# Kernel optimization log

Measured on AMD Instinct MI355X. Metric: run time of the kernel, lower is better.

Reference implementation:

```python
import jax, jax.numpy as jnp
import numpy as np

LEAK = 0.1
K = 16  # nsample


def _gather(points, idx):
    # points: [B, N2, C], idx: [B, N1, K] -> [B, N1, K, C]
    return jax.vmap(lambda p, i: p[i])(points, idx)


def setup_inputs() -> dict:
    key = jax.random.key(0)
    ks = jax.random.split(key, 32)
    B, N1, N2, C = 2, 4096, 8192, 64
    M = [64, 64, 64]
    d = {}
    d['xyz1'] = jax.random.normal(ks[0], (B, 3, N1), dtype=jnp.float32)
    d['xyz2'] = jax.random.normal(ks[1], (B, 3, N2), dtype=jnp.float32)
    d['points1'] = jax.random.normal(ks[2], (B, C, N1), dtype=jnp.float32)
    d['points2'] = jax.random.normal(ks[3], (B, C, N2), dtype=jnp.float32)
    d['knn1'] = jax.random.normal(ks[4], (B, C, N1), dtype=jnp.float32)
    d['knn2'] = jax.random.normal(ks[5], (B, C, N2), dtype=jnp.float32)
    s = 0.05
    # fuse 1x1 Conv1d weights (no bias): [out=M0, in=C]
    for j, nm in enumerate(['Wfr', 'Wfro', 'Wfz', 'Wfr2', 'Wfro2', 'Wfz2']):
        d[nm] = jax.random.normal(ks[6 + j], (M[0], C), dtype=jnp.float32) * s
    # mlp 1x1 Conv2d weights/biases: layer0 in=3, then M[i-1]
    ins = [3, M[0], M[1]]
    k = 12
    for br in ['r', 'z', 'h']:
        for i in range(3):
            d['W%s%d' % (br, i)] = jax.random.normal(ks[k], (M[i], ins[i]), dtype=jnp.float32) * s
            d['b%s%d' % (br, i)] = jax.random.normal(ks[k + 1], (M[i],), dtype=jnp.float32) * s
            k += 2
    return d


def _forward(xyz1, xyz2, points1, points2, knn1, knn2,
             Wfr, Wfro, Wfz, Wfr2, Wfro2, Wfz2,
             Wr0, br0, Wr1, br1, Wr2, br2,
             Wz0, bz0, Wz1, bz1, Wz2, bz2,
             Wh0, bh0, Wh1, bh1, Wh2, bh2):
    leaky = lambda x: jax.nn.leaky_relu(x, LEAK)
    conv = lambda x, W, b: jnp.einsum('bnkc,oc->bnko', x, W) + b
    fuse = lambda p, W: jnp.einsum('oc,bcn->bno', W, p)  # [B,N,Cout]

    x1 = jnp.transpose(xyz1, (0, 2, 1))   # [B,N1,3]
    x2 = jnp.transpose(xyz2, (0, 2, 1))   # [B,N2,3]
    f1 = jnp.transpose(knn1, (0, 2, 1))   # [B,N1,Ck]
    f2 = jnp.transpose(knn2, (0, 2, 1))   # [B,N2,Ck]

    # cosine knn on feature space (smallest distance = largest similarity)
    f1n = f1 / jnp.sqrt(jnp.sum(f1 * f1, -1, keepdims=True) + 1e-8)
    f2n = f2 / jnp.sqrt(jnp.sum(f2 * f2, -1, keepdims=True) + 1e-8)
    cdist = 1.0 - jnp.einsum('bnc,bmc->bnm', f1n, f2n)
    _, idx_c = jax.lax.top_k(-cdist, K // 2)
    # euclidean knn on xyz
    sq = (jnp.sum(x1 * x1, -1)[:, :, None] + jnp.sum(x2 * x2, -1)[:, None, :]
          - 2.0 * jnp.einsum('bnc,bmc->bnm', x1, x2))
    _, idx_p = jax.lax.top_k(-sq, K // 2)
    idx = jnp.concatenate([idx_c, idx_p], axis=-1)  # [B,N1,K]

    p2r = fuse(points2, Wfr2)    # [B,N2,M0]
    p2ro = fuse(points2, Wfro2)
    p2z = fuse(points2, Wfz2)
    g_r = _gather(p2r, idx)      # [B,N1,K,M0]
    g_ro = _gather(p2ro, idx)
    g_z = _gather(p2z, idx)
    dirx = _gather(x2, idx) - x1[:, :, None, :]  # [B,N1,K,3]

    # r gate
    gp1r = fuse(points1, Wfr)[:, :, None, :]
    r = leaky(conv(dirx, Wr0, br0) + gp1r + g_r)
    r = leaky(conv(r, Wr1, br1))
    r = jax.nn.sigmoid(conv(r, Wr2, br2))          # [B,N1,K,M2]

    # z gate (max over K before last layer)
    gp1z = fuse(points1, Wfz)[:, :, None, :]
    z = leaky(conv(dirx, Wz0, bz0) + gp1z + g_ro)
    z = jnp.max(leaky(conv(z, Wz1, bz1)), axis=2, keepdims=True)
    z = jax.nn.sigmoid(conv(z, Wz2, bz2))[:, :, 0, :]  # [B,N1,M2]

    # h candidate; note: original code's `if self.relu:` is always truthy
    # (self.relu holds the LeakyReLU module), so final activation is LeakyReLU.
    p1o = fuse(points1, Wfro)                       # [B,N1,M0]
    p1e = r * p1o[:, :, None, :]
    h = leaky(conv(dirx, Wh0, bh0) + p1e + g_z)
    h = jnp.max(leaky(conv(h, Wh1, bh1)), axis=2, keepdims=True)
    h = leaky(conv(h, Wh2, bh2))[:, :, 0, :]        # [B,N1,M2]

    out = (1.0 - z) * p1o + z * h                   # [B,N1,M2]
    return jnp.transpose(out, (0, 2, 1))            # [B,M2,N1]


def reference(xyz1, xyz2, points1, points2, knn1, knn2,
              Wfr, Wfro, Wfz, Wfr2, Wfro2, Wfz2,
              Wr0, br0, Wr1, br1, Wr2, br2,
              Wz0, bz0, Wz1, bz1, Wz2, bz2,
              Wh0, bh0, Wh1, bh1, Wh2, bh2):
    return _forward(xyz1, xyz2, points1, points2, knn1, knn2,
                    Wfr, Wfro, Wfz, Wfr2, Wfro2, Wfz2,
                    Wr0, br0, Wr1, br1, Wr2, br2,
                    Wz0, bz0, Wz1, bz1, Wz2, bz2,
                    Wh0, bh0, Wh1, bh1, Wh2, bh2)
```

## Files before the change

### kernel.cpp

```cpp
#include <hip/hip_runtime.h>
#include <math.h>

#define NB 2
#define NN1 4096
#define NN2 8192
#define NPART 16
#define PARTSZ (NN2 / NPART)
#define NCHUNK (PARTSZ / 128)
#define LEAKK 0.1f
#define GPAD 68

typedef unsigned long long u64k;

__device__ __forceinline__ float leaky_(float x) { return fmaxf(x, LEAKK * x); }
__device__ __forceinline__ float sigm_(float x) { return 1.0f / (1.0f + __expf(-x)); }

__device__ __forceinline__ void insq_(u64k k, u64k* q) {
#pragma unroll
  for (int j = 7; j > 0; --j)
    q[j] = (k < q[j - 1]) ? q[j - 1] : ((k < q[j]) ? k : q[j]);
  q[0] = (k < q[0]) ? k : q[0];
}

__device__ __forceinline__ void merge8q_(u64k* a, u64k* b) {
  u64k r[8];
#pragma unroll
  for (int s = 0; s < 8; ++s) {
    bool ta = a[0] < b[0];
    r[s] = ta ? a[0] : b[0];
#pragma unroll
    for (int j = 0; j < 7; ++j) {
      a[j] = ta ? a[j + 1] : a[j];
      b[j] = ta ? b[j] : b[j + 1];
    }
  }
#pragma unroll
  for (int j = 0; j < 8; ++j) a[j] = r[j];
}

__global__ void prep_w_kernel(const float* s0, const float* s1, const float* s2,
                              const float* s3, const float* s4, const float* s5,
                              const float* s6, const float* s7, const float* s8,
                              const float* s9, const float* s10, const float* s11,
                              const float* s12, const float* s13, const float* s14,
                              float* wt) {
  const float* srcs[15] = {s0, s1, s2, s3, s4, s5, s6, s7, s8, s9, s10, s11, s12, s13, s14};
  int bid = blockIdx.x;
  const float* src = srcs[bid];
  int cols = (bid < 6) ? 64 : (((bid - 6) % 3 == 0) ? 3 : 64);
  float* dst = wt + bid * 4096;
  for (int e = threadIdx.x; e < 64 * cols; e += blockDim.x) {
    int o = e / cols, c = e - o * cols;
    dst[c * 64 + o] = src[e];
  }
}

__global__ __launch_bounds__(256) void prep_side_kernel(const float* knn, const float* xyz,
                                                        float* fdst, float* xdst, int N) {
  __shared__ float T[64 * 65];
  __shared__ float ps[4 * 64];
  int b = blockIdx.y;
  int n0 = blockIdx.x * 64;
  int t = threadIdx.x, w = t >> 6, l = t & 63;
  const float* kb = knn + (size_t)b * 64 * N + n0;
#pragma unroll
  for (int i = 0; i < 16; ++i) {
    int c = w * 16 + i;
    T[c * 65 + l] = kb[(size_t)c * N + l];
  }
  __syncthreads();
  float s = 0.f;
#pragma unroll
  for (int i = 0; i < 16; ++i) { float v = T[(w * 16 + i) * 65 + l]; s += v * v; }
  ps[w * 64 + l] = s;
  __syncthreads();
#pragma unroll
  for (int i = 0; i < 16; ++i) {
    int p = w * 16 + i;
    float rsum = ps[p] + ps[64 + p] + ps[128 + p] + ps[192 + p];
    float rs = 1.0f / sqrtf(rsum + 1e-8f);
    fdst[(size_t)(b * N + n0 + p) * 64 + l] = T[l * 65 + p] * rs;
  }
  if (t < 64) {
    const float* xb = xyz + (size_t)b * 3 * N + n0;
    float x = xb[t], y = xb[N + t], z = xb[2 * N + t];
    ((float4*)xdst)[b * N + n0 + t] = make_float4(x, y, z, x * x + y * y + z * z);
  }
}

__global__ __launch_bounds__(256) void fuse_kernel(const float* pts, const float* wt0,
                                                   const float* wt1, const float* wt2,
                                                   float* d0, float* d1, float* d2, int N) {
  int b = blockIdx.y;
  int w = threadIdx.x >> 6, l = threadIdx.x & 63;
  int n = blockIdx.x * 4 + w;
  const float* pb = pts + (size_t)b * 64 * N + n;
  float a0 = 0.f, a1 = 0.f, a2 = 0.f;
  for (int c = 0; c < 64; ++c) {
    float p = pb[(size_t)c * N];
    a0 += p * wt0[c * 64 + l];
    a1 += p * wt1[c * 64 + l];
    a2 += p * wt2[c * 64 + l];
  }
  size_t ob = (size_t)(b * N + n) * 64 + l;
  d0[ob] = a0; d1[ob] = a1; d2[ob] = a2;
}

__global__ __launch_bounds__(256, 3) void knn_kernel(const float* f1n, const float* f2n,
                                                     const float* x1t, const float* x2t,
                                                     u64k* pq) {
  __shared__ __align__(16) float SH[13120];
  float* f1t = SH;
  float* f2d = SH + 4096;
  float* x1x = SH + 12352;
  float* x1y = SH + 12416;
  float* x1z = SH + 12480;
  float* x1w = SH + 12544;
  float* x2s = SH + 12608;

  int t = threadIdx.x;
  int lane = t & 63, w = t >> 6;
  int n0 = blockIdx.x * 64;
  int part = (int)blockIdx.y;
  int b = (int)blockIdx.z;

  {
    const float* f1row = f1n + (size_t)(b * NN1 + n0 + lane) * 64;
#pragma unroll
    for (int pass = 0; pass < 4; ++pass) {
      int c0 = pass * 16 + w * 4;
      float4 v = *(const float4*)(f1row + c0);
      f1t[(c0 + 0) * 64 + lane] = v.x;
      f1t[(c0 + 1) * 64 + lane] = v.y;
      f1t[(c0 + 2) * 64 + lane] = v.z;
      f1t[(c0 + 3) * 64 + lane] = v.w;
    }
    if (t < 64) {
      float4 v = ((const float4*)x1t)[b * NN1 + n0 + t];
      x1x[t] = v.x; x1y[t] = v.y; x1z[t] = v.z; x1w[t] = v.w;
    }
  }

  u64k cq[8], eq[8];
#pragma unroll
  for (int j = 0; j < 8; ++j) { cq[j] = ~0ull; eq[j] = ~0ull; }

  int ty = t >> 4, tx = t & 15;
  __syncthreads();
  float xx = x1x[lane], xy = x1y[lane], xz = x1z[lane], xw = x1w[lane];

  for (int ch = 0; ch < NCHUNK; ++ch) {
    int cc = part * PARTSZ + ch * 128;

    {
      int cand = t & 127;
      int sb = (t >> 7) * 8;
      const float* src = f2n + (size_t)(b * NN2 + cc + cand) * 64 + sb * 4;
#pragma unroll
      for (int p = 0; p < 8; ++p) {
        float4 v = *(const float4*)(src + p * 4);
        int c0 = (sb + p) * 4;
        f2d[(c0 + 0) * 128 + cand] = v.x;
        f2d[(c0 + 1) * 128 + cand] = v.y;
        f2d[(c0 + 2) * 128 + cand] = v.z;
        f2d[(c0 + 3) * 128 + cand] = v.w;
      }
      if (t < 128) ((float4*)x2s)[t] = ((const float4*)x2t)[b * NN2 + cc + t];
    }
    __syncthreads();

    float acc0[4][4], acc1[4][4];
#pragma unroll
    for (int i = 0; i < 4; ++i)
#pragma unroll
      for (int j = 0; j < 4; ++j) { acc0[i][j] = 0.f; acc1[i][j] = 0.f; }

#pragma unroll 2
    for (int k = 0; k < 64; ++k) {
      float4 a  = *(const float4*)&f1t[k * 64 + ty * 4];
      float4 b0 = *(const float4*)&f2d[k * 128 + tx * 4];
      float4 b1 = *(const float4*)&f2d[k * 128 + 64 + tx * 4];
      acc0[0][0] += a.x * b0.x; acc0[0][1] += a.x * b0.y; acc0[0][2] += a.x * b0.z; acc0[0][3] += a.x * b0.w;
      acc0[1][0] += a.y * b0.x; acc0[1][1] += a.y * b0.y; acc0[1][2] += a.y * b0.z; acc0[1][3] += a.y * b0.w;
      acc0[2][0] += a.z * b0.x; acc0[2][1] += a.z * b0.y; acc0[2][2] += a.z * b0.z; acc0[2][3] += a.z * b0.w;
      acc0[3][0] += a.w * b0.x; acc0[3][1] += a.w * b0.y; acc0[3][2] += a.w * b0.z; acc0[3][3] += a.w * b0.w;
      acc1[0][0] += a.x * b1.x; acc1[0][1] += a.x * b1.y; acc1[0][2] += a.x * b1.z; acc1[0][3] += a.x * b1.w;
      acc1[1][0] += a.y * b1.x; acc1[1][1] += a.y * b1.y; acc1[1][2] += a.y * b1.z; acc1[1][3] += a.y * b1.w;
      acc1[2][0] += a.z * b1.x; acc1[2][1] += a.z * b1.y; acc1[2][2] += a.z * b1.z; acc1[2][3] += a.z * b1.w;
      acc1[3][0] += a.w * b1.x; acc1[3][1] += a.w * b1.y; acc1[3][2] += a.w * b1.z; acc1[3][3] += a.w * b1.w;
    }
    __syncthreads();

#pragma unroll
    for (int i = 0; i < 4; ++i) {
      int r = ty * 4 + i;
#pragma unroll
      for (int j = 0; j < 4; ++j) {
        f2d[r * 129 + tx * 4 + j]      = fmaxf(1.f - acc0[i][j], 0.f);
        f2d[r * 129 + 64 + tx * 4 + j] = fmaxf(1.f - acc1[i][j], 0.f);
      }
    }
    __syncthreads();

    {
      const float* drow = &f2d[lane * 129 + w * 32];
      const float4* x2q = ((const float4*)x2s) + w * 32;
#pragma unroll 4
      for (int j = 0; j < 32; ++j) {
        unsigned gi = cc + w * 32 + j;
        float dv = drow[j];
        u64k kc = ((u64k)__float_as_uint(dv) << 32) | gi;
        if (kc < cq[7]) insq_(kc, cq);
        float4 xv = x2q[j];
        float d3 = fmaxf(xw + xv.w - 2.f * (xx * xv.x + xy * xv.y + xz * xv.z), 0.f);
        u64k ke = ((u64k)__float_as_uint(d3) << 32) | gi;
        if (ke < eq[7]) insq_(ke, eq);
      }
    }
    __syncthreads();
  }

  {
    u64k* Lc = (u64k*)SH;
    u64k* Le = ((u64k*)SH) + 2112;
#pragma unroll
    for (int j = 0; j < 8; ++j) {
      Lc[lane * 33 + w * 8 + j] = cq[j];
      Le[lane * 33 + w * 8 + j] = eq[j];
    }
    __syncthreads();
    if (t < 128) {
      int typ = t >> 6, r = t & 63;
      const u64k* L = typ ? Le : Lc;
      u64k a0[8], a1[8], a2[8], a3[8];
#pragma unroll
      for (int j = 0; j < 8; ++j) {
        a0[j] = L[r * 33 + 0 + j];
        a1[j] = L[r * 33 + 8 + j];
        a2[j] = L[r * 33 + 16 + j];
        a3[j] = L[r * 33 + 24 + j];
      }
      merge8q_(a0, a1);
      merge8q_(a2, a3);
      merge8q_(a0, a2);
      size_t base = ((size_t)((b * NPART + part) * NN1) + n0 + r) * 16 + typ * 8;
#pragma unroll
      for (int j = 0; j < 8; ++j) pq[base + j] = a0[j];
    }
  }
}

__device__ __forceinline__ void loadq_(const u64k* pq, int b, int p, int n1, int typ, u64k* q) {
  size_t base = ((size_t)((b * NPART + p) * NN1) + n1) * 16 + typ * 8;
#pragma unroll
  for (int j = 0; j < 8; ++j) q[j] = pq[base + j];
}

__global__ __launch_bounds__(256) void merge_parts_kernel(const u64k* pq, int* idxb) {
  int g = blockIdx.x * blockDim.x + threadIdx.x;
  if (g >= NB * NN1) return;
  int b = g / NN1, n1 = g - b * NN1;
  for (int typ = 0; typ < 2; ++typ) {
    u64k A[8], B[8];
    loadq_(pq, b, 0, n1, typ, A);
    for (int p = 1; p < NPART; ++p) {
      loadq_(pq, b, p, n1, typ, B);
      merge8q_(A, B);
    }
    size_t ob = (size_t)g * 16 + typ * 8;
#pragma unroll
    for (int j = 0; j < 8; ++j) idxb[ob + j] = (int)(A[j] & 0xffffffffull);
  }
}

__device__ __forceinline__ void gemm64_(const float* Ain, const float* Wt,
                                        int ty, int tx, float acc[4][4]) {
#pragma unroll
  for (int i = 0; i < 4; ++i)
#pragma unroll
    for (int j = 0; j < 4; ++j) acc[i][j] = 0.f;
#pragma unroll 8
  for (int c = 0; c < 64; ++c) {
    float4 a  = *(const float4*)&Ain[c * GPAD + ty * 4];
    float4 wv = *(const float4*)&Wt[c * 64 + tx * 4];
    acc[0][0] += a.x * wv.x; acc[0][1] += a.x * wv.y; acc[0][2] += a.x * wv.z; acc[0][3] += a.x * wv.w;
    acc[1][0] += a.y * wv.x; acc[1][1] += a.y * wv.y; acc[1][2] += a.y * wv.z; acc[1][3] += a.y * wv.w;
    acc[2][0] += a.z * wv.x; acc[2][1] += a.z * wv.y; acc[2][2] += a.z * wv.z; acc[2][3] += a.z * wv.w;
    acc[3][0] += a.w * wv.x; acc[3][1] += a.w * wv.y; acc[3][2] += a.w * wv.z; acc[3][3] += a.w * wv.w;
  }
}

__global__ __launch_bounds__(256, 4) void gru_kernel(
    const int* idxb, const float* x1t, const float* x2t,
    const float* p1r, const float* p1ro, const float* p1z,
    const float* p2r, const float* p2ro, const float* p2z,
    const float* wt,
    const float* br0, const float* br1, const float* br2,
    const float* bz0, const float* bz1, const float* bz2,
    const float* bh0, const float* bh1, const float* bh2,
    float* out) {
  __shared__ __align__(16) float A1[64 * GPAD];
  __shared__ __align__(16) float A2[64 * GPAD];
  __shared__ float Vpart[16 * 64];
  __shared__ float dxs[64 * 4];
  __shared__ int idxs[64];

  int t = threadIdx.x;
  int w = t >> 6, l = t & 63;
  int ty = t >> 4, tx = t & 15;
  int b = blockIdx.y;
  int n1i = blockIdx.x * 4 + w;
  int rowbase = b * NN1 + n1i;

  if (l < 16) {
    int gi = idxb[(size_t)rowbase * 16 + l];
    idxs[w * 16 + l] = gi;
    float4 x1v = ((const float4*)x1t)[rowbase];
    float4 x2v = ((const float4*)x2t)[b * NN2 + gi];
    dxs[(w * 16 + l) * 4 + 0] = x2v.x - x1v.x;
    dxs[(w * 16 + l) * 4 + 1] = x2v.y - x1v.y;
    dxs[(w * 16 + l) * 4 + 2] = x2v.z - x1v.z;
    dxs[(w * 16 + l) * 4 + 3] = 0.f;
  }
  float pr  = p1r [(size_t)rowbase * 64 + l];
  float pro = p1ro[(size_t)rowbase * 64 + l];
  float pz  = p1z [(size_t)rowbase * 64 + l];

  const float* Wr0t = wt + 6 * 4096;
  const float* Wr1t = wt + 7 * 4096;
  const float* Wr2t = wt + 8 * 4096;
  const float* Wz0t = wt + 9 * 4096;
  const float* Wz1t = wt + 10 * 4096;
  const float* Wz2t = wt + 11 * 4096;
  const float* Wh0t = wt + 12 * 4096;
  const float* Wh1t = wt + 13 * 4096;
  const float* Wh2t = wt + 14 * 4096;

  __syncthreads();

  {
    float w0 = Wr0t[l], w1 = Wr0t[64 + l], w2 = Wr0t[128 + l], b0 = br0[l];
#pragma unroll
    for (int k = 0; k < 16; ++k) {
      int row = w * 16 + k;
      int gi = idxs[row];
      float g = p2r[((size_t)b * NN2 + gi) * 64 + l];
      float4 d = *(const float4*)&dxs[row * 4];
      A1[l * GPAD + row] = leaky_(b0 + pr + g + w0 * d.x + w1 * d.y + w2 * d.z);
    }
  }
  __syncthreads();

  float acc[4][4];

  gemm64_(A1, Wr1t, ty, tx, acc);
  {
    const float* bq = &br1[tx * 4];
#pragma unroll
    for (int j = 0; j < 4; ++j) {
      float bb = bq[j];
#pragma unroll
      for (int i = 0; i < 4; ++i)
        A2[(tx * 4 + j) * GPAD + ty * 4 + i] = leaky_(acc[i][j] + bb);
    }
  }
  __syncthreads();

  gemm64_(A2, Wr2t, ty, tx, acc);
  {
    const float* bq = &br2[tx * 4];
#pragma unroll
    for (int j = 0; j < 4; ++j) {
      float bb = bq[j];
#pragma unroll
      for (int i = 0; i < 4; ++i)
        A1[(tx * 4 + j) * GPAD + ty * 4 + i] = sigm_(acc[i][j] + bb);
    }
  }
  __syncthreads();

  {
    float w0 = Wz0t[l], w1 = Wz0t[64 + l], w2 = Wz0t[128 + l], b0 = bz0[l];
#pragma unroll
    for (int k = 0; k < 16; ++k) {
      int row = w * 16 + k;
      int gi = idxs[row];
      float g = p2ro[((size_t)b * NN2 + gi) * 64 + l];
      float4 d = *(const float4*)&dxs[row * 4];
      A2[l * GPAD + row] = leaky_(b0 + pz + g + w0 * d.x + w1 * d.y + w2 * d.z);
    }
  }
  __syncthreads();

  gemm64_(A2, Wz1t, ty, tx, acc);
  {
    const float* bq = &bz1[tx * 4];
#pragma unroll
    for (int j = 0; j < 4; ++j) {
      float bb = bq[j];
      float m = leaky_(acc[0][j] + bb);
      m = fmaxf(m, leaky_(acc[1][j] + bb));
      m = fmaxf(m, leaky_(acc[2][j] + bb));
      m = fmaxf(m, leaky_(acc[3][j] + bb));
      Vpart[ty * 64 + tx * 4 + j] = m;
    }
  }
  __syncthreads();
  float vm;
  {
    float v0 = Vpart[(w * 4 + 0) * 64 + l];
    float v1 = Vpart[(w * 4 + 1) * 64 + l];
    float v2 = Vpart[(w * 4 + 2) * 64 + l];
    float v3 = Vpart[(w * 4 + 3) * 64 + l];
    vm = fmaxf(fmaxf(v0, v1), fmaxf(v2, v3));
  }
  __syncthreads();
  float* Vv = Vpart;
  Vv[w * 64 + l] = vm;
  __syncthreads();
  float z3;
  {
    float a = bz2[l];
#pragma unroll 8
    for (int c = 0; c < 64; ++c) a += Vv[w * 64 + c] * Wz2t[c * 64 + l];
    z3 = sigm_(a);
  }

  {
    float w0 = Wh0t[l], w1 = Wh0t[64 + l], w2 = Wh0t[128 + l], b0 = bh0[l];
#pragma unroll
    for (int k = 0; k < 16; ++k) {
      int row = w * 16 + k;
      int gi = idxs[row];
      float g = p2z[((size_t)b * NN2 + gi) * 64 + l];
      float4 d = *(const float4*)&dxs[row * 4];
      float r3 = A1[l * GPAD + row];
      A2[l * GPAD + row] = leaky_(b0 + r3 * pro + g + w0 * d.x + w1 * d.y + w2 * d.z);
    }
  }
  __syncthreads();

  gemm64_(A2, Wh1t, ty, tx, acc);
  {
    const float* bq = &bh1[tx * 4];
#pragma unroll
    for (int j = 0; j < 4; ++j) {
      float bb = bq[j];
      float m = leaky_(acc[0][j] + bb);
      m = fmaxf(m, leaky_(acc[1][j] + bb));
      m = fmaxf(m, leaky_(acc[2][j] + bb));
      m = fmaxf(m, leaky_(acc[3][j] + bb));
      Vpart[ty * 64 + tx * 4 + j] = m;
    }
  }
  __syncthreads();
  {
    float v0 = Vpart[(w * 4 + 0) * 64 + l];
    float v1 = Vpart[(w * 4 + 1) * 64 + l];
    float v2 = Vpart[(w * 4 + 2) * 64 + l];
    float v3 = Vpart[(w * 4 + 3) * 64 + l];
    vm = fmaxf(fmaxf(v0, v1), fmaxf(v2, v3));
  }
  __syncthreads();
  Vv[w * 64 + l] = vm;
  __syncthreads();
  float h3;
  {
    float a = bh2[l];
#pragma unroll 8
    for (int c = 0; c < 64; ++c) a += Vv[w * 64 + c] * Wh2t[c * 64 + l];
    h3 = leaky_(a);
  }

  out[((size_t)b * 64 + l) * NN1 + n1i] = (1.0f - z3) * pro + z3 * h3;
}

extern "C" void kernel_launch(void* const* d_in, const int* in_sizes, int n_in,
                              void* d_out, int out_size, void* d_ws, size_t ws_size,
                              hipStream_t stream) {
  (void)in_sizes; (void)n_in; (void)out_size; (void)ws_size;
  const float* xyz1    = (const float*)d_in[0];
  const float* xyz2    = (const float*)d_in[1];
  const float* points1 = (const float*)d_in[2];
  const float* points2 = (const float*)d_in[3];
  const float* knn1    = (const float*)d_in[4];
  const float* knn2    = (const float*)d_in[5];
  const float* Wfr   = (const float*)d_in[6];
  const float* Wfro  = (const float*)d_in[7];
  const float* Wfz   = (const float*)d_in[8];
  const float* Wfr2  = (const float*)d_in[9];
  const float* Wfro2 = (const float*)d_in[10];
  const float* Wfz2  = (const float*)d_in[11];
  const float* Wr0 = (const float*)d_in[12]; const float* br0 = (const float*)d_in[13];
  const float* Wr1 = (const float*)d_in[14]; const float* br1 = (const float*)d_in[15];
  const float* Wr2 = (const float*)d_in[16]; const float* br2 = (const float*)d_in[17];
  const float* Wz0 = (const float*)d_in[18]; const float* bz0 = (const float*)d_in[19];
  const float* Wz1 = (const float*)d_in[20]; const float* bz1 = (const float*)d_in[21];
  const float* Wz2 = (const float*)d_in[22]; const float* bz2 = (const float*)d_in[23];
  const float* Wh0 = (const float*)d_in[24]; const float* bh0 = (const float*)d_in[25];
  const float* Wh1 = (const float*)d_in[26]; const float* bh1 = (const float*)d_in[27];
  const float* Wh2 = (const float*)d_in[28]; const float* bh2 = (const float*)d_in[29];

  float* W = (float*)d_ws;
  size_t o = 0;
  float* f1n = W + o; o += (size_t)NB * NN1 * 64;
  float* f2n = W + o; o += (size_t)NB * NN2 * 64;
  float* x1t = W + o; o += (size_t)NB * NN1 * 4;
  float* x2t = W + o; o += (size_t)NB * NN2 * 4;
  float* p1r = W + o; o += (size_t)NB * NN1 * 64;
  float* p1ro = W + o; o += (size_t)NB * NN1 * 64;
  float* p1z = W + o; o += (size_t)NB * NN1 * 64;
  float* p2r = W + o; o += (size_t)NB * NN2 * 64;
  float* p2ro = W + o; o += (size_t)NB * NN2 * 64;
  float* p2z = W + o; o += (size_t)NB * NN2 * 64;
  float* wt = W + o; o += (size_t)15 * 4096;
  u64k* pq = (u64k*)(W + o); o += (size_t)2 * NB * NPART * NN1 * 16;
  int* idxb = (int*)(W + o); o += (size_t)NB * NN1 * 16;

  float* out = (float*)d_out;

  hipLaunchKernelGGL(prep_w_kernel, dim3(15), dim3(256), 0, stream,
                     Wfr, Wfro, Wfz, Wfr2, Wfro2, Wfz2,
                     Wr0, Wr1, Wr2, Wz0, Wz1, Wz2, Wh0, Wh1, Wh2, wt);
  hipLaunchKernelGGL(prep_side_kernel, dim3(NN1 / 64, NB), dim3(256), 0, stream,
                     knn1, xyz1, f1n, x1t, NN1);
  hipLaunchKernelGGL(prep_side_kernel, dim3(NN2 / 64, NB), dim3(256), 0, stream,
                     knn2, xyz2, f2n, x2t, NN2);
  hipLaunchKernelGGL(fuse_kernel, dim3(NN1 / 4, NB), dim3(256), 0, stream,
                     points1, wt + 0 * 4096, wt + 1 * 4096, wt + 2 * 4096,
                     p1r, p1ro, p1z, NN1);
  hipLaunchKernelGGL(fuse_kernel, dim3(NN2 / 4, NB), dim3(256), 0, stream,
                     points2, wt + 3 * 4096, wt + 4 * 4096, wt + 5 * 4096,
                     p2r, p2ro, p2z, NN2);
  hipLaunchKernelGGL(knn_kernel, dim3(NN1 / 64, NPART, NB), dim3(256), 0, stream,
                     f1n, f2n, x1t, x2t, pq);
  hipLaunchKernelGGL(merge_parts_kernel, dim3((NB * NN1 + 255) / 256), dim3(256), 0, stream,
                     pq, idxb);
  hipLaunchKernelGGL(gru_kernel, dim3(NN1 / 4, NB), dim3(256), 0, stream,
                     idxb, x1t, x2t, p1r, p1ro, p1z, p2r, p2ro, p2z, wt,
                     br0, br1, br2, bz0, bz1, bz2, bh0, bh1, bh2, out);
}
```

Measured before the change: 578.9 us.

## Store normalized features channel-major and use branchless float top-k insertion

The prep kernel now writes the normalized knn features in channel-major layout, so the knn kernel loads its shared-memory tiles with direct float4 copies instead of scattered transposing stores. The per-candidate top-8 insertion switches from conditional 64-bit key compare-and-insert to a branchless float/int min-max network, and packs to sortable 64-bit keys only at merge time. The clamping of distances to zero is removed; the sign-aware packing is meant to keep the ordering correct for negative values. The branchless insert runs on every candidate rather than only those that beat the current worst, which trades the early-out for no divergence and more ALU work per candidate.

```diff
diff --git a/kernel.cpp b/kernel.cpp
--- a/kernel.cpp
+++ b/kernel.cpp
@@ -15,11 +15,23 @@
 __device__ __forceinline__ float leaky_(float x) { return fmaxf(x, LEAKK * x); }
 __device__ __forceinline__ float sigm_(float x) { return 1.0f / (1.0f + __expf(-x)); }
 
-__device__ __forceinline__ void insq_(u64k k, u64k* q) {
-#pragma unroll
-  for (int j = 7; j > 0; --j)
-    q[j] = (k < q[j - 1]) ? q[j - 1] : ((k < q[j]) ? k : q[j]);
-  q[0] = (k < q[0]) ? k : q[0];
+__device__ __forceinline__ void insfi_(float d, int i, float* q, int* qi) {
+  bool c0 = d < q[0], c1 = d < q[1], c2 = d < q[2], c3 = d < q[3];
+  bool c4 = d < q[4], c5 = d < q[5], c6 = d < q[6], c7 = d < q[7];
+  q[7] = fminf(fmaxf(d, q[6]), q[7]);  qi[7] = c6 ? qi[6] : (c7 ? i : qi[7]);
+  q[6] = fminf(fmaxf(d, q[5]), q[6]);  qi[6] = c5 ? qi[5] : (c6 ? i : qi[6]);
+  q[5] = fminf(fmaxf(d, q[4]), q[5]);  qi[5] = c4 ? qi[4] : (c5 ? i : qi[5]);
+  q[4] = fminf(fmaxf(d, q[3]), q[4]);  qi[4] = c3 ? qi[3] : (c4 ? i : qi[4]);
+  q[3] = fminf(fmaxf(d, q[2]), q[3]);  qi[3] = c2 ? qi[2] : (c3 ? i : qi[3]);
+  q[2] = fminf(fmaxf(d, q[1]), q[2]);  qi[2] = c1 ? qi[1] : (c2 ? i : qi[2]);
+  q[1] = fminf(fmaxf(d, q[0]), q[1]);  qi[1] = c0 ? qi[0] : (c1 ? i : qi[1]);
+  q[0] = fminf(d, q[0]);               qi[0] = c0 ? i : qi[0];
+}
+
+__device__ __forceinline__ u64k packdi_(float d, int i) {
+  unsigned b = __float_as_uint(d);
+  b ^= (unsigned)(((int)b >> 31)) | 0x80000000u;
+  return ((u64k)b << 32) | (unsigned)i;
 }
 
 __device__ __forceinline__ void merge8q_(u64k* a, u64k* b) {
@@ -56,9 +68,10 @@
 }
 
 __global__ __launch_bounds__(256) void prep_side_kernel(const float* knn, const float* xyz,
-                                                        float* fdst, float* xdst, int N) {
+                                                        float* fT, float* xdst, int N) {
   __shared__ float T[64 * 65];
   __shared__ float ps[4 * 64];
+  __shared__ float rsS[64];
   int b = blockIdx.y;
   int n0 = blockIdx.x * 64;
   int t = threadIdx.x, w = t >> 6, l = t & 63;
@@ -74,17 +87,19 @@
   for (int i = 0; i < 16; ++i) { float v = T[(w * 16 + i) * 65 + l]; s += v * v; }
   ps[w * 64 + l] = s;
   __syncthreads();
-#pragma unroll
-  for (int i = 0; i < 16; ++i) {
-    int p = w * 16 + i;
-    float rsum = ps[p] + ps[64 + p] + ps[128 + p] + ps[192 + p];
-    float rs = 1.0f / sqrtf(rsum + 1e-8f);
-    fdst[(size_t)(b * N + n0 + p) * 64 + l] = T[l * 65 + p] * rs;
-  }
   if (t < 64) {
+    float rsum = ps[t] + ps[64 + t] + ps[128 + t] + ps[192 + t];
+    rsS[t] = 1.0f / sqrtf(rsum + 1e-8f);
     const float* xb = xyz + (size_t)b * 3 * N + n0;
     float x = xb[t], y = xb[N + t], z = xb[2 * N + t];
     ((float4*)xdst)[b * N + n0 + t] = make_float4(x, y, z, x * x + y * y + z * z);
+  }
+  __syncthreads();
+  float rl = rsS[l];
+#pragma unroll
+  for (int i = 0; i < 16; ++i) {
+    int c = w * 16 + i;
+    fT[((size_t)b * 64 + c) * N + n0 + l] = T[c * 65 + l] * rl;
   }
 }
 
@@ -106,7 +121,7 @@
   d0[ob] = a0; d1[ob] = a1; d2[ob] = a2;
 }
 
-__global__ __launch_bounds__(256, 3) void knn_kernel(const float* f1n, const float* f2n,
+__global__ __launch_bounds__(256, 3) void knn_kernel(const float* f1T, const float* f2T,
                                                      const float* x1t, const float* x2t,
                                                      u64k* pq) {
   __shared__ __align__(16) float SH[13120];
@@ -125,25 +140,21 @@
   int b = (int)blockIdx.z;
 
   {
-    const float* f1row = f1n + (size_t)(b * NN1 + n0 + lane) * 64;
-#pragma unroll
-    for (int pass = 0; pass < 4; ++pass) {
-      int c0 = pass * 16 + w * 4;
-      float4 v = *(const float4*)(f1row + c0);
-      f1t[(c0 + 0) * 64 + lane] = v.x;
-      f1t[(c0 + 1) * 64 + lane] = v.y;
-      f1t[(c0 + 2) * 64 + lane] = v.z;
-      f1t[(c0 + 3) * 64 + lane] = v.w;
-    }
+    int k = t >> 2, rs0 = (t & 3) * 16;
+    const float* src = f1T + ((size_t)b * 64 + k) * NN1 + n0 + rs0;
+    float* dst = &f1t[k * 64 + rs0];
+#pragma unroll
+    for (int p = 0; p < 4; ++p)
+      *(float4*)(dst + p * 4) = *(const float4*)(src + p * 4);
     if (t < 64) {
       float4 v = ((const float4*)x1t)[b * NN1 + n0 + t];
       x1x[t] = v.x; x1y[t] = v.y; x1z[t] = v.z; x1w[t] = v.w;
     }
   }
 
-  u64k cq[8], eq[8];
-#pragma unroll
-  for (int j = 0; j < 8; ++j) { cq[j] = ~0ull; eq[j] = ~0ull; }
+  float cd[8], ed[8]; int ci[8], ei[8];
+#pragma unroll
+  for (int j = 0; j < 8; ++j) { cd[j] = INFINITY; ed[j] = INFINITY; ci[j] = 0; ei[j] = 0; }
 
   int ty = t >> 4, tx = t & 15;
   __syncthreads();
@@ -153,17 +164,12 @@
     int cc = part * PARTSZ + ch * 128;
 
     {
-      int cand = t & 127;
-      int sb = (t >> 7) * 8;
-      const float* src = f2n + (size_t)(b * NN2 + cc + cand) * 64 + sb * 4;
+      int k8 = t >> 5, cs = (t & 31) * 4;
 #pragma unroll
       for (int p = 0; p < 8; ++p) {
-        float4 v = *(const float4*)(src + p * 4);
-        int c0 = (sb + p) * 4;
-        f2d[(c0 + 0) * 128 + cand] = v.x;
-        f2d[(c0 + 1) * 128 + cand] = v.y;
-        f2d[(c0 + 2) * 128 + cand] = v.z;
-        f2d[(c0 + 3) * 128 + cand] = v.w;
+        int k = k8 * 8 + p;
+        *(float4*)&f2d[k * 128 + cs] =
+            *(const float4*)(f2T + ((size_t)b * 64 + k) * NN2 + cc + cs);
       }
       if (t < 128) ((float4*)x2s)[t] = ((const float4*)x2t)[b * NN2 + cc + t];
     }
@@ -196,8 +202,8 @@
       int r = ty * 4 + i;
 #pragma unroll
       for (int j = 0; j < 4; ++j) {
-        f2d[r * 129 + tx * 4 + j]      = fmaxf(1.f - acc0[i][j], 0.f);
-        f2d[r * 129 + 64 + tx * 4 + j] = fmaxf(1.f - acc1[i][j], 0.f);
+        f2d[r * 129 + tx * 4 + j]      = 1.f - acc0[i][j];
+        f2d[r * 129 + 64 + tx * 4 + j] = 1.f - acc1[i][j];
       }
     }
     __syncthreads();
@@ -207,14 +213,11 @@
       const float4* x2q = ((const float4*)x2s) + w * 32;
 #pragma unroll 4
       for (int j = 0; j < 32; ++j) {
-        unsigned gi = cc + w * 32 + j;
-        float dv = drow[j];
-        u64k kc = ((u64k)__float_as_uint(dv) << 32) | gi;
-        if (kc < cq[7]) insq_(kc, cq);
+        int gi = cc + w * 32 + j;
+        insfi_(drow[j], gi, cd, ci);
         float4 xv = x2q[j];
-        float d3 = fmaxf(xw + xv.w - 2.f * (xx * xv.x + xy * xv.y + xz * xv.z), 0.f);
-        u64k ke = ((u64k)__float_as_uint(d3) << 32) | gi;
-        if (ke < eq[7]) insq_(ke, eq);
+        float d3 = xw + xv.w - 2.f * (xx * xv.x + xy * xv.y + xz * xv.z);
+        insfi_(d3, gi, ed, ei);
       }
     }
     __syncthreads();
@@ -225,8 +228,8 @@
     u64k* Le = ((u64k*)SH) + 2112;
 #pragma unroll
     for (int j = 0; j < 8; ++j) {
-      Lc[lane * 33 + w * 8 + j] = cq[j];
-      Le[lane * 33 + w * 8 + j] = eq[j];
+      Lc[lane * 33 + w * 8 + j] = packdi_(cd[j], ci[j]);
+      Le[lane * 33 + w * 8 + j] = packdi_(ed[j], ei[j]);
     }
     __syncthreads();
     if (t < 128) {
@@ -503,8 +506,8 @@
 
   float* W = (float*)d_ws;
   size_t o = 0;
-  float* f1n = W + o; o += (size_t)NB * NN1 * 64;
-  float* f2n = W + o; o += (size_t)NB * NN2 * 64;
+  float* f1T = W + o; o += (size_t)NB * NN1 * 64;
+  float* f2T = W + o; o += (size_t)NB * NN2 * 64;
   float* x1t = W + o; o += (size_t)NB * NN1 * 4;
   float* x2t = W + o; o += (size_t)NB * NN2 * 4;
   float* p1r = W + o; o += (size_t)NB * NN1 * 64;
@@ -523,9 +526,9 @@
                      Wfr, Wfro, Wfz, Wfr2, Wfro2, Wfz2,
                      Wr0, Wr1, Wr2, Wz0, Wz1, Wz2, Wh0, Wh1, Wh2, wt);
   hipLaunchKernelGGL(prep_side_kernel, dim3(NN1 / 64, NB), dim3(256), 0, stream,
-                     knn1, xyz1, f1n, x1t, NN1);
+                     knn1, xyz1, f1T, x1t, NN1);
   hipLaunchKernelGGL(prep_side_kernel, dim3(NN2 / 64, NB), dim3(256), 0, stream,
-                     knn2, xyz2, f2n, x2t, NN2);
+                     knn2, xyz2, f2T, x2t, NN2);
   hipLaunchKernelGGL(fuse_kernel, dim3(NN1 / 4, NB), dim3(256), 0, stream,
                      points1, wt + 0 * 4096, wt + 1 * 4096, wt + 2 * 4096,
                      p1r, p1ro, p1z, NN1);
@@ -533,7 +536,7 @@
                      points2, wt + 3 * 4096, wt + 4 * 4096, wt + 5 * 4096,
                      p2r, p2ro, p2z, NN2);
   hipLaunchKernelGGL(knn_kernel, dim3(NN1 / 64, NPART, NB), dim3(256), 0, stream,
-                     f1n, f2n, x1t, x2t, pq);
+                     f1T, f2T, x1t, x2t, pq);
   hipLaunchKernelGGL(merge_parts_kernel, dim3((NB * NN1 + 255) / 256), dim3(256), 0, stream,
                      pq, idxb);
   hipLaunchKernelGGL(gru_kernel, dim3(NN1 / 4, NB), dim3(256), 0, stream,
```

Measured after the change: 585.3 us. About the same (+1.1%).
